# Performance work log

Measured on AMD Instinct MI355X. Metric: run time of the kernel, lower is better.

Reference implementation:

```python
import jax, jax.numpy as jnp
import numpy as np

INPUT_DIM = 512
OUTPUT_DIM = 32
DEGREE = 8


def setup_inputs() -> dict:
    key = jax.random.key(0)
    kx, kw = jax.random.split(key)
    x = jax.random.normal(kx, (65536, INPUT_DIM), dtype=jnp.float32)
    # xavier_normal_ on [input_dim, output_dim, degree+1]: torch treats last dims as fan;
    # fan_in = output_dim*(degree+1), fan_out = input_dim*(degree+1)
    fan_in = OUTPUT_DIM * (DEGREE + 1)
    fan_out = INPUT_DIM * (DEGREE + 1)
    std = float(np.sqrt(2.0 / (fan_in + fan_out)))
    cheby_coeffs = std * jax.random.normal(kw, (INPUT_DIM, OUTPUT_DIM, DEGREE + 1), dtype=jnp.float32)
    return {"x": x, "cheby_coeffs": cheby_coeffs}


def reference(x, cheby_coeffs):
    xt = jnp.tanh(x.reshape(-1, INPUT_DIM))
    T = [jnp.ones_like(xt), 2.0 * xt]
    for n in range(2, DEGREE + 1):
        T.append(2.0 * xt * T[n - 1] - T[n - 2])
    T = jnp.stack(T, axis=-1)  # [B, I, degree+1]
    y = jnp.einsum('bij,ioj->bo', T, cheby_coeffs)  # [B, O]
    return y
```

## Files before the change

### kernel.cpp

```cpp
#include <hip/hip_runtime.h>
#include <hip/hip_fp16.h>


typedef _Float16 half8 __attribute__((ext_vector_type(8)));
typedef float float4v __attribute__((ext_vector_type(4)));

#define N_ROWS   65536
#define N_I      512
#define N_O      32
#define N_CHUNKS 16
#define STEPS    8
#define CHUNK_F16 8192

__global__ void pack_b(const float* __restrict__ coeffs, _Float16* __restrict__ bsw) {
    int id = blockIdx.x * blockDim.x + threadIdx.x;
    if (id >= 128 * 2 * 64 * 8) return;
    int jj = id & 7;
    int L  = (id >> 3) & 63;
    int t  = (id >> 9) & 1;
    int s  = id >> 10;
    int ci = s >> 3, sl = s & 7;
    int j  = sl + 1;
    int ii = ((L >> 4) << 3) + jj;
    int i  = ci * 32 + ii;
    int o  = t * 16 + (L & 15);
    bsw[id] = (_Float16)coeffs[(i * 32 + o) * 9 + j];
}

__global__ void bias_k(const float* __restrict__ coeffs, float* __restrict__ bias) {
    int o = blockIdx.x;
    int t = threadIdx.x;
    float s = 0.f;
    for (int i = t; i < N_I; i += 64) s += coeffs[(i * 32 + o) * 9 + 0];
    for (int off = 32; off; off >>= 1) s += __shfl_down(s, off, 64);
    if (t == 0) bias[o] = s;
}

__device__ __forceinline__ float fast_tanh(float v) {
    float e = __expf(2.0f * v);
    return __builtin_fmaf(-2.0f, __builtin_amdgcn_rcpf(e + 1.0f), 1.0f);
}

__global__ __launch_bounds__(256, 2) void cheby_main(
        const float* __restrict__ x, const _Float16* __restrict__ bsw,
        const float* __restrict__ bias, float* __restrict__ y) {
    __shared__ __align__(16) _Float16 bl[2][CHUNK_F16];

    const int tid = threadIdx.x;
    const int wv  = tid >> 6;
    const int L   = tid & 63;
    const int q   = L >> 4;
    const int mr  = L & 15;
    const int m0  = blockIdx.x * 128 + wv * 32;
    const int r0  = m0 + mr;
    const int r1  = r0 + 16;

    {
        const uint4* src = (const uint4*)bsw;
        uint4* dst = (uint4*)&bl[0][0];
#pragma unroll
        for (int it = 0; it < 4; ++it) dst[it * 256 + tid] = src[it * 256 + tid];
    }

    float4v acc[2][2];
#pragma unroll
    for (int a = 0; a < 2; ++a)
#pragma unroll
        for (int b = 0; b < 2; ++b)
#pragma unroll
            for (int e = 0; e < 4; ++e) acc[a][b][e] = 0.f;

    for (int ci = 0; ci < N_CHUNKS; ++ci) {
        __syncthreads();
        const int buf = ci & 1;
        if (ci < N_CHUNKS - 1) {
            const uint4* src = (const uint4*)(bsw + (ci + 1) * CHUNK_F16);
            uint4* dst = (uint4*)&bl[buf ^ 1][0];
#pragma unroll
            for (int it = 0; it < 4; ++it) dst[it * 256 + tid] = src[it * 256 + tid];
        }

        const int i0 = ci * 32 + q * 8;
        const float4v xa = *(const float4v*)(x + (size_t)r0 * N_I + i0);
        const float4v xb = *(const float4v*)(x + (size_t)r0 * N_I + i0 + 4);
        const float4v xc = *(const float4v*)(x + (size_t)r1 * N_I + i0);
        const float4v xd = *(const float4v*)(x + (size_t)r1 * N_I + i0 + 4);

        float w0[8], w1[8], up0[8], uc0[8], up1[8], uc1[8];
#pragma unroll
        for (int e = 0; e < 4; ++e) {
            w0[e]     = 2.0f * fast_tanh(xa[e]);
            w0[e + 4] = 2.0f * fast_tanh(xb[e]);
            w1[e]     = 2.0f * fast_tanh(xc[e]);
            w1[e + 4] = 2.0f * fast_tanh(xd[e]);
        }
#pragma unroll
        for (int e = 0; e < 8; ++e) {
            up0[e] = 1.0f; uc0[e] = w0[e];
            up1[e] = 1.0f; uc1[e] = w1[e];
        }

#pragma unroll
        for (int s = 0; s < STEPS; ++s) {
            half8 a0, a1;
#pragma unroll
            for (int e = 0; e < 8; ++e) {
                a0[e] = (_Float16)uc0[e];
                a1[e] = (_Float16)uc1[e];
            }
            const half8 b0 = *(const half8*)&bl[buf][(s * 2 + 0) * 512 + L * 8];
            const half8 b1 = *(const half8*)&bl[buf][(s * 2 + 1) * 512 + L * 8];
            acc[0][0] = __builtin_amdgcn_mfma_f32_16x16x32_f16(a0, b0, acc[0][0], 0, 0, 0);
            acc[0][1] = __builtin_amdgcn_mfma_f32_16x16x32_f16(a0, b1, acc[0][1], 0, 0, 0);
            acc[1][0] = __builtin_amdgcn_mfma_f32_16x16x32_f16(a1, b0, acc[1][0], 0, 0, 0);
            acc[1][1] = __builtin_amdgcn_mfma_f32_16x16x32_f16(a1, b1, acc[1][1], 0, 0, 0);
#pragma unroll
            for (int e = 0; e < 8; ++e) {
                float n0 = __builtin_fmaf(w0[e], uc0[e], -up0[e]);
                float n1 = __builtin_fmaf(w1[e], uc1[e], -up1[e]);
                up0[e] = uc0[e]; uc0[e] = n0;
                up1[e] = uc1[e]; uc1[e] = n1;
            }
        }
    }

    const float b_n0 = bias[mr];
    const float b_n1 = bias[16 + mr];
#pragma unroll
    for (int mt = 0; mt < 2; ++mt) {
#pragma unroll
        for (int e = 0; e < 4; ++e) {
            const int r = m0 + mt * 16 + q * 4 + e;
            y[(size_t)r * N_O + mr]      = acc[mt][0][e] + b_n0;
            y[(size_t)r * N_O + 16 + mr] = acc[mt][1][e] + b_n1;
        }
    }
}

extern "C" void kernel_launch(void* const* d_in, const int* in_sizes, int n_in,
                              void* d_out, int out_size, void* d_ws, size_t ws_size,
                              hipStream_t stream) {
    const float* x      = (const float*)d_in[0];
    const float* coeffs = (const float*)d_in[1];
    float* yout = (float*)d_out;

    _Float16* bsw = (_Float16*)d_ws;
    float* bias   = (float*)((char*)d_ws + 131072 * sizeof(_Float16));

    pack_b<<<512, 256, 0, stream>>>(coeffs, bsw);
    bias_k<<<32, 64, 0, stream>>>(coeffs, bias);
    cheby_main<<<512, 256, 0, stream>>>(x, bsw, bias, yout);
}
```

Baseline: 200.4 us.

## Drop LDS staging, read B fragments from global, prefetch x, merge prep kernels

The main kernel becomes single-wave blocks of 64 threads, 2048 in total. Each wave loads its B fragments straight from global/L2 into registers instead of staging them through double-buffered shared memory, which removes the __syncthreads barriers. The next chunk of x is loaded while the current chunk is processed, and the fp16 conversion uses packed cvt_pkrtz. The pack and bias kernels are merged into one launch. In exchange, the 256 KB of B is re-read from cache by every wave, which raises L2 traffic and register pressure.

```diff
diff --git a/kernel.cpp b/kernel.cpp
--- a/kernel.cpp
+++ b/kernel.cpp
@@ -3,18 +3,26 @@
 
 
 typedef _Float16 half8 __attribute__((ext_vector_type(8)));
+typedef __fp16  fp16x2 __attribute__((ext_vector_type(2)));
 typedef float float4v __attribute__((ext_vector_type(4)));
 
-#define N_ROWS   65536
-#define N_I      512
-#define N_O      32
+#define N_I 512
+#define N_O 32
 #define N_CHUNKS 16
-#define STEPS    8
+#define STEPS 8
 #define CHUNK_F16 8192
 
-__global__ void pack_b(const float* __restrict__ coeffs, _Float16* __restrict__ bsw) {
-    int id = blockIdx.x * blockDim.x + threadIdx.x;
-    if (id >= 128 * 2 * 64 * 8) return;
+__global__ void prep(const float* __restrict__ coeffs, _Float16* __restrict__ bsw,
+                     float* __restrict__ bias) {
+    if (blockIdx.x == 512) {
+        int o = threadIdx.x >> 3, p = threadIdx.x & 7;
+        float s = 0.f;
+        for (int i = p; i < N_I; i += 8) s += coeffs[(i * 32 + o) * 9];
+        for (int off = 4; off; off >>= 1) s += __shfl_down(s, off, 8);
+        if (p == 0) bias[o] = s;
+        return;
+    }
+    int id = blockIdx.x * 256 + threadIdx.x;
     int jj = id & 7;
     int L  = (id >> 3) & 63;
     int t  = (id >> 9) & 1;
@@ -27,40 +35,34 @@
     bsw[id] = (_Float16)coeffs[(i * 32 + o) * 9 + j];
 }
 
-__global__ void bias_k(const float* __restrict__ coeffs, float* __restrict__ bias) {
-    int o = blockIdx.x;
-    int t = threadIdx.x;
-    float s = 0.f;
-    for (int i = t; i < N_I; i += 64) s += coeffs[(i * 32 + o) * 9 + 0];
-    for (int off = 32; off; off >>= 1) s += __shfl_down(s, off, 64);
-    if (t == 0) bias[o] = s;
-}
-
 __device__ __forceinline__ float fast_tanh(float v) {
     float e = __expf(2.0f * v);
     return __builtin_fmaf(-2.0f, __builtin_amdgcn_rcpf(e + 1.0f), 1.0f);
 }
 
-__global__ __launch_bounds__(256, 2) void cheby_main(
+__device__ __forceinline__ half8 pack8(const float* u) {
+    union { fp16x2 h[4]; half8 v; } r;
+    r.h[0] = __builtin_amdgcn_cvt_pkrtz(u[0], u[1]);
+    r.h[1] = __builtin_amdgcn_cvt_pkrtz(u[2], u[3]);
+    r.h[2] = __builtin_amdgcn_cvt_pkrtz(u[4], u[5]);
+    r.h[3] = __builtin_amdgcn_cvt_pkrtz(u[6], u[7]);
+    return r.v;
+}
+
+__global__ __launch_bounds__(64) void cheby_main(
         const float* __restrict__ x, const _Float16* __restrict__ bsw,
         const float* __restrict__ bias, float* __restrict__ y) {
-    __shared__ __align__(16) _Float16 bl[2][CHUNK_F16];
+    const int L  = threadIdx.x;
+    const int q  = L >> 4;
+    const int mr = L & 15;
+    const int m0 = blockIdx.x * 32;
+    const float* xr0 = x + (size_t)(m0 + mr) * N_I + q * 8;
+    const float* xr1 = xr0 + 16 * N_I;
 
-    const int tid = threadIdx.x;
-    const int wv  = tid >> 6;
-    const int L   = tid & 63;
-    const int q   = L >> 4;
-    const int mr  = L & 15;
-    const int m0  = blockIdx.x * 128 + wv * 32;
-    const int r0  = m0 + mr;
-    const int r1  = r0 + 16;
-
-    {
-        const uint4* src = (const uint4*)bsw;
-        uint4* dst = (uint4*)&bl[0][0];
-#pragma unroll
-        for (int it = 0; it < 4; ++it) dst[it * 256 + tid] = src[it * 256 + tid];
-    }
+    float4v xa = *(const float4v*)(xr0);
+    float4v xb = *(const float4v*)(xr0 + 4);
+    float4v xc = *(const float4v*)(xr1);
+    float4v xd = *(const float4v*)(xr1 + 4);
 
     float4v acc[2][2];
 #pragma unroll
@@ -70,21 +72,15 @@
 #pragma unroll
             for (int e = 0; e < 4; ++e) acc[a][b][e] = 0.f;
 
+    const _Float16* bc = bsw + L * 8;
+
     for (int ci = 0; ci < N_CHUNKS; ++ci) {
-        __syncthreads();
-        const int buf = ci & 1;
-        if (ci < N_CHUNKS - 1) {
-            const uint4* src = (const uint4*)(bsw + (ci + 1) * CHUNK_F16);
-            uint4* dst = (uint4*)&bl[buf ^ 1][0];
+        half8 bf[STEPS][2];
 #pragma unroll
-            for (int it = 0; it < 4; ++it) dst[it * 256 + tid] = src[it * 256 + tid];
+        for (int s = 0; s < STEPS; ++s) {
+            bf[s][0] = *(const half8*)(bc + ci * CHUNK_F16 + (s * 2 + 0) * 512);
+            bf[s][1] = *(const half8*)(bc + ci * CHUNK_F16 + (s * 2 + 1) * 512);
         }
-
-        const int i0 = ci * 32 + q * 8;
-        const float4v xa = *(const float4v*)(x + (size_t)r0 * N_I + i0);
-        const float4v xb = *(const float4v*)(x + (size_t)r0 * N_I + i0 + 4);
-        const float4v xc = *(const float4v*)(x + (size_t)r1 * N_I + i0);
-        const float4v xd = *(const float4v*)(x + (size_t)r1 * N_I + i0 + 4);
 
         float w0[8], w1[8], up0[8], uc0[8], up1[8], uc1[8];
 #pragma unroll
@@ -100,20 +96,22 @@
             up1[e] = 1.0f; uc1[e] = w1[e];
         }
 
+        if (ci < N_CHUNKS - 1) {
+            const int o = (ci + 1) * 32;
+            xa = *(const float4v*)(xr0 + o);
+            xb = *(const float4v*)(xr0 + o + 4);
+            xc = *(const float4v*)(xr1 + o);
+            xd = *(const float4v*)(xr1 + o + 4);
+        }
+
 #pragma unroll
         for (int s = 0; s < STEPS; ++s) {
-            half8 a0, a1;
-#pragma unroll
-            for (int e = 0; e < 8; ++e) {
-                a0[e] = (_Float16)uc0[e];
-                a1[e] = (_Float16)uc1[e];
-            }
-            const half8 b0 = *(const half8*)&bl[buf][(s * 2 + 0) * 512 + L * 8];
-            const half8 b1 = *(const half8*)&bl[buf][(s * 2 + 1) * 512 + L * 8];
-            acc[0][0] = __builtin_amdgcn_mfma_f32_16x16x32_f16(a0, b0, acc[0][0], 0, 0, 0);
-            acc[0][1] = __builtin_amdgcn_mfma_f32_16x16x32_f16(a0, b1, acc[0][1], 0, 0, 0);
-            acc[1][0] = __builtin_amdgcn_mfma_f32_16x16x32_f16(a1, b0, acc[1][0], 0, 0, 0);
-            acc[1][1] = __builtin_amdgcn_mfma_f32_16x16x32_f16(a1, b1, acc[1][1], 0, 0, 0);
+            const half8 a0 = pack8(uc0);
+            const half8 a1 = pack8(uc1);
+            acc[0][0] = __builtin_amdgcn_mfma_f32_16x16x32_f16(a0, bf[s][0], acc[0][0], 0, 0, 0);
+            acc[0][1] = __builtin_amdgcn_mfma_f32_16x16x32_f16(a0, bf[s][1], acc[0][1], 0, 0, 0);
+            acc[1][0] = __builtin_amdgcn_mfma_f32_16x16x32_f16(a1, bf[s][0], acc[1][0], 0, 0, 0);
+            acc[1][1] = __builtin_amdgcn_mfma_f32_16x16x32_f16(a1, bf[s][1], acc[1][1], 0, 0, 0);
 #pragma unroll
             for (int e = 0; e < 8; ++e) {
                 float n0 = __builtin_fmaf(w0[e], uc0[e], -up0[e]);
@@ -147,7 +145,6 @@
     _Float16* bsw = (_Float16*)d_ws;
     float* bias   = (float*)((char*)d_ws + 131072 * sizeof(_Float16));
 
-    pack_b<<<512, 256, 0, stream>>>(coeffs, bsw);
-    bias_k<<<32, 64, 0, stream>>>(coeffs, bias);
-    cheby_main<<<512, 256, 0, stream>>>(x, bsw, bias, yout);
+    prep<<<513, 256, 0, stream>>>(coeffs, bsw, bias);
+    cheby_main<<<2048, 64, 0, stream>>>(x, bsw, bias, yout);
 }
```

Result: slower. 224.9 us (+12.2%).
